# Kernel optimization log

Hardware: AMD Instinct MI355X
Metric: run time of the kernel (lower is better)

Reference implementation:

```python
import jax, jax.numpy as jnp
import numpy as np

EPS = 1e-5
NUM_HEADS = 8

def _inorm(x):
    # InstanceNorm1d (affine=False): normalize over last (length) axis per (B, C)
    m = x.mean(axis=-1, keepdims=True)
    v = x.var(axis=-1, keepdims=True)  # biased variance, as torch instance norm
    return (x - m) * jax.lax.rsqrt(v + EPS)

def setup_inputs() -> dict:
    key = jax.random.key(0)
    ks = jax.random.split(key, 12)
    B, Nl, HW = 4, 1024, 4096
    Cl, Cv, Ck, Cval, Cout = 512, 512, 256, 256, 256
    w = lambda k, shape: (jax.random.normal(k, shape, jnp.float32) * 0.02)
    return {
        "l": jax.random.normal(ks[0], (B, Nl, Cl), jnp.float32),
        "x": jax.random.normal(ks[1], (B, HW, Cv), jnp.float32),
        "Wq": w(ks[2], (Ck, Cl)),   "bq": w(ks[3], (Ck,)),
        "Wk": w(ks[4], (Ck, Cv)),   "bk": w(ks[5], (Ck,)),
        "Wv": w(ks[6], (Cval, Cv)), "bv": w(ks[7], (Cval,)),
        "Ww": w(ks[8], (Cout, Cval)), "bw": w(ks[9], (Cout,)),
    }

def reference(l, x, Wq, bq, Wk, bk, Wv, bv, Ww, bw):
    H = NUM_HEADS
    Ck = Wq.shape[0]
    Cv = Wv.shape[0]
    dk, dv = Ck // H, Cv // H
    B, Nl, _ = l.shape
    HW = x.shape[1]

    # 1x1 Conv1d == per-position linear
    q = jnp.einsum('blc,kc->blk', l, Wq) + bq                     # [B, Nl, Ck]
    k = jnp.einsum('bnc,kc->bkn', x, Wk) + bk[None, :, None]      # [B, Ck, HW]
    k = _inorm(k)                                                  # InstanceNorm over HW
    v = jnp.einsum('bnc,kc->bkn', x, Wv) + bv[None, :, None]      # [B, Cv, HW]

    q = q.reshape(B, Nl, H, dk).transpose(0, 2, 1, 3)             # [B, H, Nl, dk]
    k = k.reshape(B, H, dk, HW)                                   # [B, H, dk, HW]
    v = v.reshape(B, H, dv, HW)                                   # [B, H, dv, HW]

    sim = jnp.einsum('bhld,bhdn->bhln', q, k) * (Ck ** -0.5)      # [B, H, Nl, HW]
    att = jax.nn.softmax(sim, axis=-1)
    out = jnp.einsum('bhln,bhdn->bhld', att, v)                   # [B, H, Nl, dv]

    out = out.transpose(0, 2, 1, 3).reshape(B, Nl, Cv)            # [B, Nl, Cv]
    out = jnp.einsum('blc,oc->bol', out, Ww) + bw[None, :, None]  # [B, Cout, Nl]
    out = _inorm(out)                                              # InstanceNorm over Nl
    return out.transpose(0, 2, 1)                                  # [B, Nl, Cout]
```

## Files before the change

### kernel.cpp

```cpp
#include <hip/hip_runtime.h>

constexpr int Bn = 4, NL = 1024, HWn = 4096, NH = 8;

typedef __attribute__((ext_vector_type(8))) short bf16x8;
typedef __attribute__((ext_vector_type(4))) float f32x4;
#define MFMA16 __builtin_amdgcn_mfma_f32_16x16x32_bf16

extern "C" __device__ float __ocml_native_exp2_f32(float);

__device__ __forceinline__ float b2f(unsigned short u) {
  union { unsigned int i; float f; } x; x.i = ((unsigned int)u) << 16; return x.f;
}
__device__ __forceinline__ unsigned short f2b(float f) {
  union { float f; unsigned int i; } x; x.f = f;
  unsigned int r = x.i + 0x7fffu + ((x.i >> 16) & 1u);
  return (unsigned short)(r >> 16);
}

__device__ __forceinline__ void async_load16(const unsigned short* g, unsigned short* l) {
  __builtin_amdgcn_global_load_lds(
      (const __attribute__((address_space(1))) unsigned int*)g,
      (__attribute__((address_space(3))) unsigned int*)l, 16, 0, 0);
}

__global__ __launch_bounds__(256) void conv_bf16(const float* __restrict__ src,
    unsigned short* __restrict__ dst, int n)
{
  int i = (blockIdx.x * 256 + threadIdx.x) * 4;
  if (i < n) {
    float4 v = *(const float4*)(src + i);
    ushort4 o; o.x = f2b(v.x); o.y = f2b(v.y); o.z = f2b(v.z); o.w = f2b(v.w);
    *(ushort4*)(dst + i) = o;
  }
}

__global__ __launch_bounds__(256) void conv_w4(const float* __restrict__ Wk,
    const float* __restrict__ Wv, const float* __restrict__ Wq,
    const float* __restrict__ Ww,
    unsigned short* __restrict__ wkb, unsigned short* __restrict__ wvb,
    unsigned short* __restrict__ wqb,
    unsigned short* __restrict__ wwh, unsigned short* __restrict__ wwl)
{
  int i = (blockIdx.x * 256 + threadIdx.x) * 4;
  if (blockIdx.y == 3) {
    if (i >= 65536) return;
    float4 v = *(const float4*)(Ww + i);
    ushort4 hi, lo;
    hi.x = f2b(v.x); lo.x = f2b(v.x - b2f(hi.x));
    hi.y = f2b(v.y); lo.y = f2b(v.y - b2f(hi.y));
    hi.z = f2b(v.z); lo.z = f2b(v.z - b2f(hi.z));
    hi.w = f2b(v.w); lo.w = f2b(v.w - b2f(hi.w));
    *(ushort4*)(wwh + i) = hi;
    *(ushort4*)(wwl + i) = lo;
    return;
  }
  const float* src = blockIdx.y == 0 ? Wk : (blockIdx.y == 1 ? Wv : Wq);
  unsigned short* dst = blockIdx.y == 0 ? wkb : (blockIdx.y == 1 ? wvb : wqb);
  float4 v = *(const float4*)(src + i);
  ushort4 o; o.x = f2b(v.x); o.y = f2b(v.y); o.z = f2b(v.z); o.w = f2b(v.w);
  *(ushort4*)(dst + i) = o;
}

__global__ __launch_bounds__(256, 3) void gemm128(
    const unsigned short* __restrict__ xbf, const unsigned short* __restrict__ lbf,
    const unsigned short* __restrict__ wkb, const unsigned short* __restrict__ wvb,
    const unsigned short* __restrict__ wqb,
    const float* __restrict__ bk, const float* __restrict__ bv, const float* __restrict__ bq,
    unsigned short* __restrict__ khb, unsigned short* __restrict__ vhb,
    unsigned short* __restrict__ qbuf)
{
  __shared__ unsigned short As[2][4096];
  __shared__ unsigned short Bs[2][4096];
  const int id = blockIdx.x;
  const int mode = id < 256 ? 0 : (id < 512 ? 1 : 2);
  const int local = id - (mode == 0 ? 0 : (mode == 1 ? 256 : 512));
  const int rb = local >> 1, cb = local & 1;
  const int m0 = rb * 128, n0 = cb * 128;
  const unsigned short* A = (mode == 2) ? lbf : xbf;
  const unsigned short* W = (mode == 0) ? wkb : (mode == 1 ? wvb : wqb);
  const float* bias = (mode == 0) ? bk : (mode == 1 ? bv : bq);

  const int tid = threadIdx.x, w = tid >> 6, lane = tid & 63;
  const int quad = lane >> 4, l15 = lane & 15;
  const int wr = w >> 1, wc = w & 1;

  const int p0 = tid, p1 = tid + 256;
  const int am0 = p0 >> 2, ak0 = (p0 & 3) * 8;
  const int am1 = p1 >> 2, ak1 = (p1 & 3) * 8;

  f32x4 acc[4][4];
#pragma unroll
  for (int i = 0; i < 4; ++i)
#pragma unroll
    for (int j = 0; j < 4; ++j) acc[i][j] = (f32x4){0.f, 0.f, 0.f, 0.f};

  async_load16(A + (size_t)(m0 + am0) * 512 + ak0, &As[0][p0 * 8]);
  async_load16(A + (size_t)(m0 + am1) * 512 + ak1, &As[0][p1 * 8]);
  async_load16(W + (size_t)(n0 + am0) * 512 + ak0, &Bs[0][p0 * 8]);
  async_load16(W + (size_t)(n0 + am1) * 512 + ak1, &Bs[0][p1 * 8]);

  for (int kt = 0; kt < 16; ++kt) {
    const int cur = kt & 1;
    __syncthreads();
    if (kt < 15) {
      int k0 = (kt + 1) * 32;
      async_load16(A + (size_t)(m0 + am0) * 512 + k0 + ak0, &As[cur ^ 1][p0 * 8]);
      async_load16(A + (size_t)(m0 + am1) * 512 + k0 + ak1, &As[cur ^ 1][p1 * 8]);
      async_load16(W + (size_t)(n0 + am0) * 512 + k0 + ak0, &Bs[cur ^ 1][p0 * 8]);
      async_load16(W + (size_t)(n0 + am1) * 512 + k0 + ak1, &Bs[cur ^ 1][p1 * 8]);
    }
    bf16x8 af[4], bf[4];
#pragma unroll
    for (int fr = 0; fr < 4; ++fr)
      af[fr] = *(const bf16x8*)&As[cur][(wr * 64 + fr * 16 + l15) * 32 + quad * 8];
#pragma unroll
    for (int fc = 0; fc < 4; ++fc)
      bf[fc] = *(const bf16x8*)&Bs[cur][(wc * 64 + fc * 16 + l15) * 32 + quad * 8];
#pragma unroll
    for (int fr = 0; fr < 4; ++fr)
#pragma unroll
      for (int fc = 0; fc < 4; ++fc)
        acc[fr][fc] = MFMA16(af[fr], bf[fc], acc[fr][fc], 0, 0, 0);
  }

  float bb[4];
#pragma unroll
  for (int fc = 0; fc < 4; ++fc) bb[fc] = bias[n0 + wc * 64 + fc * 16 + l15];
  unsigned short* dst = (mode == 0) ? khb : (mode == 1 ? vhb : qbuf);
#pragma unroll
  for (int fr = 0; fr < 4; ++fr) {
#pragma unroll
    for (int fc = 0; fc < 4; ++fc) {
      int col = n0 + wc * 64 + fc * 16 + l15;
#pragma unroll
      for (int r = 0; r < 4; ++r) {
        int row = m0 + wr * 64 + fr * 16 + quad * 4 + r;
        unsigned short val = f2b(acc[fr][fc][r] + bb[fc]);
        if (mode == 2) {
          dst[(size_t)row * 256 + col] = val;
        } else {
          int b = row >> 12, n = row & 4095, h = col >> 5, d = col & 31;
          dst[((size_t)(b * 8 + h) * 4096 + n) * 32 + d] = val;
        }
      }
    }
  }
}

__global__ __launch_bounds__(256) void kvstats(const unsigned short* __restrict__ khb,
    const unsigned short* __restrict__ vhb,
    float* __restrict__ ksum, float* __restrict__ kss, float* __restrict__ vcs)
{
  const int which = blockIdx.x >> 5, bh = blockIdx.x & 31, seg = blockIdx.y;
  const int t = threadIdx.x, d = t & 31, g = t >> 5;
  __shared__ float rs[256], rss[256];
  if (which == 0) {
    const unsigned short* base = khb + (size_t)bh * 131072 + (size_t)seg * 512 * 32;
    float s = 0.f, ss = 0.f;
    for (int i = 0; i < 64; ++i) {
      float v = b2f(base[(size_t)(g + i * 8) * 32 + d]);
      s += v; ss += v * v;
    }
    rs[t] = s; rss[t] = ss;
    __syncthreads();
    if (t < 32) {
      float a = 0.f, b = 0.f;
      for (int g2 = 0; g2 < 8; ++g2) { a += rs[t + g2 * 32]; b += rss[t + g2 * 32]; }
      atomicAdd(&ksum[bh * 32 + t], a);
      atomicAdd(&kss[bh * 32 + t], b);
    }
  } else {
    const unsigned short* base = vhb + (size_t)bh * 131072 + (size_t)seg * 512 * 32;
    float s = 0.f;
    for (int i = 0; i < 64; ++i) s += b2f(base[(size_t)(g + i * 8) * 32 + d]);
    rs[t] = s;
    __syncthreads();
    if (t < 32) {
      float a = 0.f;
      for (int g2 = 0; g2 < 8; ++g2) a += rs[t + g2 * 32];
      vcs[seg * 1024 + bh * 32 + t] = a;
    }
  }
}

__global__ __launch_bounds__(256) void kfinal(const float* __restrict__ ksum,
    const float* __restrict__ kss, float* __restrict__ krstd)
{
  int i = blockIdx.x * 256 + threadIdx.x;
  float m = ksum[i] * (1.f / 4096.f);
  float var = kss[i] * (1.f / 4096.f) - m * m;
  krstd[i] = rsqrtf(var + 1e-5f);
}

__global__ __launch_bounds__(256) void vpack(const unsigned short* __restrict__ vh,
    unsigned short* __restrict__ vfrag)
{
  __shared__ unsigned short vt[256][42];
  const int bh = blockIdx.x >> 4, slab = blockIdx.x & 15;
  const unsigned short* src = vh + ((size_t)bh * 4096 + slab * 256) * 32;
  const int t = threadIdx.x;
#pragma unroll
  for (int i = 0; i < 4; ++i) {
    int p = i * 256 + t;
    int n = p >> 2, piece = p & 3;
    uint4 v = *(const uint4*)(src + (size_t)n * 32 + piece * 8);
    unsigned int* lrow = (unsigned int*)&vt[n][piece * 8];
    lrow[0] = v.x; lrow[1] = v.y; lrow[2] = v.z; lrow[3] = v.w;
  }
  __syncthreads();
#pragma unroll
  for (int i = 0; i < 4; ++i) {
    int op = i * 256 + t;
    int lanep = op & 63, rest = op >> 6;
    int dvt = rest & 1, kh2 = (rest >> 1) & 1, chunkl = rest >> 2;
    int lq = lanep >> 4, ll = lanep & 15;
    unsigned short o[8];
#pragma unroll
    for (int j = 0; j < 8; ++j) {
      int kappa = kh2 * 32 + lq * 8 + j;
      int nloc = (kappa >> 2) + 16 * (kappa & 3);
      o[j] = vt[chunkl * 64 + nloc][dvt * 16 + ll];
    }
    size_t dst = ((((size_t)bh * 64 + slab * 4 + chunkl) * 2 + kh2) * 2 + dvt) * 512 + lanep * 8;
    *(bf16x8*)(vfrag + dst) = *(const bf16x8*)o;
  }
}

__global__ __launch_bounds__(256, 4) void attn6(const unsigned short* __restrict__ qbuf,
    const unsigned short* __restrict__ khb, const unsigned short* __restrict__ vfrag,
    const float* __restrict__ krstd, const float* __restrict__ vcs,
    float* __restrict__ po, float* __restrict__ pd)
{
  const int bh = blockIdx.x, b = bh >> 3, h = bh & 7;
  const int lsuper = blockIdx.y, quarter = blockIdx.z;
  const int tid = threadIdx.x, w = tid >> 6, lane = tid & 63;
  const int quad = lane >> 4, l15 = lane & 15;

  __shared__ unsigned short kb_s[2][2048];
  __shared__ unsigned short vb_s[2][2048];
  __shared__ unsigned short ps[4][2][16][72];

  bf16x8 qa[2];
  {
    float fold[8];
    const float* rp = krstd + bh * 32 + quad * 8;
#pragma unroll
    for (int j = 0; j < 8; ++j) fold[j] = rp[j] * (0.0625f * 1.44269504f);
#pragma unroll
    for (int lf = 0; lf < 2; ++lf) {
      int l = lsuper * 128 + w * 32 + lf * 16 + l15;
      bf16x8 qr = *(const bf16x8*)(qbuf + ((size_t)(b * NL + l)) * 256 + h * 32 + quad * 8);
      const unsigned short* qq = (const unsigned short*)&qr;
      unsigned short tmp[8];
#pragma unroll
      for (int j = 0; j < 8; ++j) tmp[j] = f2b(b2f(qq[j]) * fold[j]);
      qa[lf] = *(const bf16x8*)tmp;
    }
  }

  float drow[2][4];
  f32x4 acc[2][2];
#pragma unroll
  for (int lf = 0; lf < 2; ++lf) {
#pragma unroll
    for (int r = 0; r < 4; ++r) drow[lf][r] = 0.f;
    acc[lf][0] = (f32x4){0.f,0.f,0.f,0.f};
    acc[lf][1] = (f32x4){0.f,0.f,0.f,0.f};
  }

  const unsigned short* kcbase = khb + (size_t)bh * 131072 + (size_t)quarter * 1024 * 32;
  const unsigned short* vcbase = vfrag + (size_t)bh * 131072 + (size_t)quarter * 16 * 2048;

  async_load16(kcbase + tid * 8, &kb_s[0][tid * 8]);
  async_load16(vcbase + tid * 8, &vb_s[0][tid * 8]);

  for (int c = 0; c < 16; ++c) {
    const int cur = c & 1;
    __syncthreads();
    if (c < 15) {
      async_load16(kcbase + (c + 1) * 2048 + tid * 8, &kb_s[cur ^ 1][tid * 8]);
      async_load16(vcbase + (c + 1) * 2048 + tid * 8, &vb_s[cur ^ 1][tid * 8]);
    }

    bf16x8 kb[4];
#pragma unroll
    for (int t = 0; t < 4; ++t)
      kb[t] = *(const bf16x8*)&kb_s[cur][(t * 16 + l15) * 32 + quad * 8];
    bf16x8 vb[4];
#pragma unroll
    for (int i = 0; i < 4; ++i)
      vb[i] = *(const bf16x8*)&vb_s[cur][i * 512 + lane * 8];

    f32x4 z = (f32x4){0.f,0.f,0.f,0.f};
#pragma unroll
    for (int lf = 0; lf < 2; ++lf) {
      f32x4 sv[4];
#pragma unroll
      for (int t = 0; t < 4; ++t) sv[t] = MFMA16(qa[lf], kb[t], z, 0, 0, 0);
#pragma unroll
      for (int r = 0; r < 4; ++r) {
        union { float f; unsigned int u; } e0, e1, e2, e3;
        float x0 = __ocml_native_exp2_f32(sv[0][r]);
        float x1 = __ocml_native_exp2_f32(sv[1][r]);
        float x2 = __ocml_native_exp2_f32(sv[2][r]);
        float x3 = __ocml_native_exp2_f32(sv[3][r]);
        drow[lf][r] += (x0 + x1) + (x2 + x3);
        e0.f = x0 - 1.0f; e1.f = x1 - 1.0f; e2.f = x2 - 1.0f; e3.f = x3 - 1.0f;
        uint2 pk;
        pk.x = (e0.u >> 16) | (e1.u & 0xFFFF0000u);
        pk.y = (e2.u >> 16) | (e3.u & 0xFFFF0000u);
        *(uint2*)&ps[w][lf][quad * 4 + r][l15 * 4] = pk;
      }
      asm volatile("s_waitcnt lgkmcnt(0)" ::: "memory");
#pragma unroll
      for (int kh2 = 0; kh2 < 2; ++kh2) {
        bf16x8 pa = *(const bf16x8*)&ps[w][lf][l15][kh2 * 32 + quad * 8];
#pragma unroll
        for (int dvt = 0; dvt < 2; ++dvt)
          acc[lf][dvt] = MFMA16(pa, vb[kh2 * 2 + dvt], acc[lf][dvt], 0, 0, 0);
      }
    }
  }

  const float* vc0 = vcs + (quarter * 2) * 1024 + bh * 32;
  const float* vc1 = vc0 + 1024;
  float cs0 = vc0[l15] + vc1[l15];
  float cs1 = vc0[16 + l15] + vc1[16 + l15];
#pragma unroll
  for (int lf = 0; lf < 2; ++lf)
#pragma unroll
    for (int r = 0; r < 4; ++r) {
      acc[lf][0][r] += cs0;
      acc[lf][1][r] += cs1;
    }

  const size_t PDo = (size_t)quarter * 32768 + (size_t)bh * 1024;
#pragma unroll
  for (int lf = 0; lf < 2; ++lf) {
#pragma unroll
    for (int r = 0; r < 4; ++r) {
      float sv = drow[lf][r];
      sv += __shfl_xor(sv, 1, 16);
      sv += __shfl_xor(sv, 2, 16);
      sv += __shfl_xor(sv, 4, 16);
      sv += __shfl_xor(sv, 8, 16);
      int l = lsuper * 128 + w * 32 + lf * 16 + quad * 4 + r;
      float2 val; val.x = acc[lf][0][r]; val.y = acc[lf][1][r];
      *(float2*)(po + (PDo + l) * 32 + l15 * 2) = val;
      if (l15 == 0) pd[PDo + l] = sv;
    }
  }
}

__global__ __launch_bounds__(256) void combine4(const float* __restrict__ po,
    const float* __restrict__ pd, unsigned short* __restrict__ aoh,
    unsigned short* __restrict__ aol)
{
  int gid = blockIdx.x * 256 + threadIdx.x;
  int dv = gid & 31, l = (gid >> 5) & (NL - 1), h = (gid >> 15) & 7, b = gid >> 18;
  int c = ((dv & 15) << 1) | (dv >> 4);
  size_t r = ((size_t)(b * 8 + h)) * 1024 + l;
  float d = 0.f, o = 0.f;
#pragma unroll
  for (int q = 0; q < 4; ++q) {
    size_t rr = (size_t)q * 32768 + r;
    d += pd[rr];
    o += po[rr * 32 + c];
  }
  o = o / d;
  unsigned short hi = f2b(o);
  size_t idx = ((size_t)(b * NL) + l) * 256 + h * 32 + dv;
  aoh[idx] = hi;
  aol[idx] = f2b(o - b2f(hi));
}

__global__ __launch_bounds__(256) void gemm_proj(
    const unsigned short* __restrict__ aoh, const unsigned short* __restrict__ aol,
    const unsigned short* __restrict__ wwh, const unsigned short* __restrict__ wwl,
    const float* __restrict__ bw, float* __restrict__ pj)
{
  __shared__ unsigned short As[64 * 32];
  __shared__ unsigned short Bs[128 * 32];
  const int bm = blockIdx.x * 64, bn = blockIdx.y * 128;
  const int tid = threadIdx.x, w = tid >> 6, lane = tid & 63;
  const int quad = lane >> 4, l15 = lane & 15;
  const int wr = w >> 1, wc = w & 1;
  const int arow = tid >> 2, apiece = (tid & 3) * 8;

  f32x4 acc[2][4];
#pragma unroll
  for (int i = 0; i < 2; ++i)
#pragma unroll
    for (int j = 0; j < 4; ++j) acc[i][j] = (f32x4){0.f, 0.f, 0.f, 0.f};

  for (int pair = 0; pair < 3; ++pair) {
    const unsigned short* A = (pair == 1) ? aol : aoh;
    const unsigned short* Bm = (pair == 2) ? wwl : wwh;
    for (int kt = 0; kt < 8; ++kt) {
      int k0 = kt * 32;
      __syncthreads();
      *(bf16x8*)&As[tid * 8] = *(const bf16x8*)(A + (size_t)(bm + arow) * 256 + k0 + apiece);
#pragma unroll
      for (int it = 0; it < 2; ++it) {
        int p = tid + it * 256;
        int brow = p >> 2, bpiece = (p & 3) * 8;
        *(bf16x8*)&Bs[p * 8] = *(const bf16x8*)(Bm + (size_t)(bn + brow) * 256 + k0 + bpiece);
      }
      __syncthreads();
      bf16x8 af[2], bf[4];
#pragma unroll
      for (int fr = 0; fr < 2; ++fr)
        af[fr] = *(const bf16x8*)&As[(wr * 32 + fr * 16 + l15) * 32 + quad * 8];
#pragma unroll
      for (int fc = 0; fc < 4; ++fc)
        bf[fc] = *(const bf16x8*)&Bs[(wc * 64 + fc * 16 + l15) * 32 + quad * 8];
#pragma unroll
      for (int fr = 0; fr < 2; ++fr)
#pragma unroll
        for (int fc = 0; fc < 4; ++fc)
          acc[fr][fc] = MFMA16(af[fr], bf[fc], acc[fr][fc], 0, 0, 0);
    }
  }

#pragma unroll
  for (int fr = 0; fr < 2; ++fr)
#pragma unroll
    for (int fc = 0; fc < 4; ++fc) {
      int col = bn + wc * 64 + fc * 16 + l15;
      float bb = bw[col];
#pragma unroll
      for (int r = 0; r < 4; ++r) {
        int row = bm + wr * 32 + fr * 16 + quad * 4 + r;
        pj[(size_t)row * 256 + col] = acc[fr][fc][r] + bb;
      }
    }
}

__global__ __launch_bounds__(256) void stats_kernel(const float* __restrict__ X,
    long batchStride, int rowsPerBlock,
    float* __restrict__ sum, float* __restrict__ sumsq)
{
  const int b = blockIdx.x, c = threadIdx.x;
  const long r0 = (long)blockIdx.y * rowsPerBlock;
  const float* base = X + (long)b * batchStride + r0 * 256 + c;
  float s = 0.f, ss = 0.f;
  for (int r = 0; r < rowsPerBlock; ++r) {
    float v = base[(long)r * 256];
    s += v; ss += v * v;
  }
  atomicAdd(&sum[b * 256 + c], s);
  atomicAdd(&sumsq[b * 256 + c], ss);
}

__global__ __launch_bounds__(256) void finalize_stats(const float* __restrict__ sum,
    const float* __restrict__ sumsq, float invR,
    float* __restrict__ mean, float* __restrict__ rstd)
{
  int i = blockIdx.x * 256 + threadIdx.x;
  float m = sum[i] * invR;
  float v = sumsq[i] * invR - m * m;
  mean[i] = m;
  rstd[i] = rsqrtf(v + 1e-5f);
}

__global__ __launch_bounds__(256) void final_out(const float* __restrict__ proj,
    const float* __restrict__ mean, const float* __restrict__ rstd,
    float* __restrict__ out)
{
  const int b = blockIdx.x, o = threadIdx.x;
  const int l1 = blockIdx.y * 16;
  const float m = mean[b * 256 + o], r = rstd[b * 256 + o];
  for (int i = 0; i < 16; ++i) {
    size_t idx = ((size_t)(b * NL + l1 + i)) * 256 + o;
    out[idx] = (proj[idx] - m) * r;
  }
}

extern "C" void kernel_launch(void* const* d_in, const int* in_sizes, int n_in,
                              void* d_out, int out_size, void* d_ws, size_t ws_size,
                              hipStream_t stream)
{
  const float* l  = (const float*)d_in[0];
  const float* x  = (const float*)d_in[1];
  const float* Wq = (const float*)d_in[2];
  const float* bq = (const float*)d_in[3];
  const float* Wk = (const float*)d_in[4];
  const float* bk = (const float*)d_in[5];
  const float* Wv = (const float*)d_in[6];
  const float* bv = (const float*)d_in[7];
  const float* Ww = (const float*)d_in[8];
  const float* bw = (const float*)d_in[9];
  float* out = (float*)d_out;

  unsigned short* up = (unsigned short*)d_ws;
  unsigned short* xbf   = up;
  unsigned short* lbf   = xbf   + 8388608;
  unsigned short* wkb   = lbf   + 2097152;
  unsigned short* wvb   = wkb   + 131072;
  unsigned short* wqb   = wvb   + 131072;
  unsigned short* qbuf  = wqb   + 131072;
  unsigned short* khb   = qbuf  + 1048576;
  unsigned short* vhb   = khb   + 4194304;
  unsigned short* vfrag = vhb   + 4194304;
  unsigned short* aoh   = vfrag + 4194304;
  unsigned short* aol   = aoh   + 1048576;
  unsigned short* wwh   = aol   + 1048576;
  unsigned short* wwl   = wwh   + 65536;
  float* F     = (float*)((char*)d_ws + 53477376);
  float* krstd = F;
  float* vcs   = krstd + 1024;
  float* po    = vcs + 8192;
  float* pd    = po + 4194304;
  float* pj    = pd + 131072;
  float* st    = pj + 1048576;
  float* ksum  = st;          float* kss   = st + 1024;
  float* psum  = st + 2048;   float* psq   = st + 3072;
  float* pmean = st + 4096;   float* prstd = st + 5120;

  hipMemsetAsync(st, 0, 4096 * sizeof(float), stream);

  dim3 blk(256);
  conv_bf16<<<8192, blk, 0, stream>>>(x,  xbf, 8388608);
  conv_bf16<<<2048, blk, 0, stream>>>(l,  lbf, 2097152);
  conv_w4<<<dim3(128, 4), blk, 0, stream>>>(Wk, Wv, Wq, Ww, wkb, wvb, wqb, wwh, wwl);
  gemm128<<<576, blk, 0, stream>>>(xbf, lbf, wkb, wvb, wqb, bk, bv, bq, khb, vhb, qbuf);
  kvstats<<<dim3(64, 8), blk, 0, stream>>>(khb, vhb, ksum, kss, vcs);
  kfinal<<<4, blk, 0, stream>>>(ksum, kss, krstd);
  vpack<<<512, blk, 0, stream>>>(vhb, vfrag);
  attn6<<<dim3(32, 8, 4), blk, 0, stream>>>(qbuf, khb, vfrag, krstd, vcs, po, pd);
  combine4<<<4096, blk, 0, stream>>>(po, pd, aoh, aol);
  gemm_proj<<<dim3(64, 2), blk, 0, stream>>>(aoh, aol, wwh, wwl, bw, pj);
  stats_kernel<<<dim3(4, 64), blk, 0, stream>>>(pj, (long)NL * 256, 16, psum, psq);
  finalize_stats<<<4, blk, 0, stream>>>(psum, psq, 1.0f / NL, pmean, prstd);
  final_out<<<dim3(4, 64), blk, 0, stream>>>(pj, pmean, prstd, out);
}
```

Measured before the change: 204.7 us.

## Fuse K/V and projection stats into GEMM epilogues; register-prefetch attention K/V

Moves the K sum/sumsq and V column-sum reductions into the gemm128 epilogue using wave shuffles and atomics, which removes the kvstats kernel and its re-read of khb/vhb. Likewise folds the output-projection instance-norm statistics into gemm_proj, removing stats_kernel. The attention kernel now loads K and V fragments straight from global memory into double-buffered registers instead of LDS with async copies and barriers. It also swizzles the P staging buffer and uses hardware packed bf16 conversion. Risks include extra atomic contention, higher register pressure in attention, and rounding differences from summing fp32 accumulators instead of bf16-rounded values.

Result: slower. 261.6 us (+27.8%).

```diff
diff --git a/kernel.cpp b/kernel.cpp
--- a/kernel.cpp
+++ b/kernel.cpp
@@ -67,7 +67,8 @@
     const unsigned short* __restrict__ wqb,
     const float* __restrict__ bk, const float* __restrict__ bv, const float* __restrict__ bq,
     unsigned short* __restrict__ khb, unsigned short* __restrict__ vhb,
-    unsigned short* __restrict__ qbuf)
+    unsigned short* __restrict__ qbuf,
+    float* __restrict__ ksum, float* __restrict__ kss, float* __restrict__ vcs)
 {
   __shared__ unsigned short As[2][4096];
   __shared__ unsigned short Bs[2][4096];
@@ -126,6 +127,35 @@
   float bb[4];
 #pragma unroll
   for (int fc = 0; fc < 4; ++fc) bb[fc] = bias[n0 + wc * 64 + fc * 16 + l15];
+
+  if (mode != 2) {
+    const int b = m0 >> 12;
+    const int seg = (m0 & 4095) >> 9;
+#pragma unroll
+    for (int fc = 0; fc < 4; ++fc) {
+      float s = 0.f, ssq = 0.f;
+#pragma unroll
+      for (int fr = 0; fr < 4; ++fr)
+#pragma unroll
+        for (int r = 0; r < 4; ++r) {
+          float v = acc[fr][fc][r] + bb[fc];
+          s += v; ssq += v * v;
+        }
+      s += __shfl_xor(s, 16); s += __shfl_xor(s, 32);
+      if (mode == 0) {
+        ssq += __shfl_xor(ssq, 16); ssq += __shfl_xor(ssq, 32);
+        if (quad == 0) {
+          int col = n0 + wc * 64 + fc * 16 + l15;
+          atomicAdd(&ksum[b * 256 + col], s);
+          atomicAdd(&kss[b * 256 + col], ssq);
+        }
+      } else if (quad == 0) {
+        int col = n0 + wc * 64 + fc * 16 + l15;
+        atomicAdd(&vcs[seg * 1024 + b * 256 + col], s);
+      }
+    }
+  }
+
   unsigned short* dst = (mode == 0) ? khb : (mode == 1 ? vhb : qbuf);
 #pragma unroll
   for (int fr = 0; fr < 4; ++fr) {
@@ -147,42 +177,6 @@
   }
 }
 
-__global__ __launch_bounds__(256) void kvstats(const unsigned short* __restrict__ khb,
-    const unsigned short* __restrict__ vhb,
-    float* __restrict__ ksum, float* __restrict__ kss, float* __restrict__ vcs)
-{
-  const int which = blockIdx.x >> 5, bh = blockIdx.x & 31, seg = blockIdx.y;
-  const int t = threadIdx.x, d = t & 31, g = t >> 5;
-  __shared__ float rs[256], rss[256];
-  if (which == 0) {
-    const unsigned short* base = khb + (size_t)bh * 131072 + (size_t)seg * 512 * 32;
-    float s = 0.f, ss = 0.f;
-    for (int i = 0; i < 64; ++i) {
-      float v = b2f(base[(size_t)(g + i * 8) * 32 + d]);
-      s += v; ss += v * v;
-    }
-    rs[t] = s; rss[t] = ss;
-    __syncthreads();
-    if (t < 32) {
-      float a = 0.f, b = 0.f;
-      for (int g2 = 0; g2 < 8; ++g2) { a += rs[t + g2 * 32]; b += rss[t + g2 * 32]; }
-      atomicAdd(&ksum[bh * 32 + t], a);
-      atomicAdd(&kss[bh * 32 + t], b);
-    }
-  } else {
-    const unsigned short* base = vhb + (size_t)bh * 131072 + (size_t)seg * 512 * 32;
-    float s = 0.f;
-    for (int i = 0; i < 64; ++i) s += b2f(base[(size_t)(g + i * 8) * 32 + d]);
-    rs[t] = s;
-    __syncthreads();
-    if (t < 32) {
-      float a = 0.f;
-      for (int g2 = 0; g2 < 8; ++g2) a += rs[t + g2 * 32];
-      vcs[seg * 1024 + bh * 32 + t] = a;
-    }
-  }
-}
-
 __global__ __launch_bounds__(256) void kfinal(const float* __restrict__ ksum,
     const float* __restrict__ kss, float* __restrict__ krstd)
 {
@@ -226,7 +220,7 @@
   }
 }
 
-__global__ __launch_bounds__(256, 4) void attn6(const unsigned short* __restrict__ qbuf,
+__global__ __launch_bounds__(256, 4) void attn7(const unsigned short* __restrict__ qbuf,
     const unsigned short* __restrict__ khb, const unsigned short* __restrict__ vfrag,
     const float* __restrict__ krstd, const float* __restrict__ vcs,
     float* __restrict__ po, float* __restrict__ pd)
@@ -236,9 +230,7 @@
   const int tid = threadIdx.x, w = tid >> 6, lane = tid & 63;
   const int quad = lane >> 4, l15 = lane & 15;
 
-  __shared__ unsigned short kb_s[2][2048];
-  __shared__ unsigned short vb_s[2][2048];
-  __shared__ unsigned short ps[4][2][16][72];
+  __shared__ unsigned short ps[4][2][16][64];
 
   bf16x8 qa[2];
   {
@@ -268,30 +260,28 @@
     acc[lf][1] = (f32x4){0.f,0.f,0.f,0.f};
   }
 
-  const unsigned short* kcbase = khb + (size_t)bh * 131072 + (size_t)quarter * 1024 * 32;
-  const unsigned short* vcbase = vfrag + (size_t)bh * 131072 + (size_t)quarter * 16 * 2048;
-
-  async_load16(kcbase + tid * 8, &kb_s[0][tid * 8]);
-  async_load16(vcbase + tid * 8, &vb_s[0][tid * 8]);
-
-  for (int c = 0; c < 16; ++c) {
-    const int cur = c & 1;
-    __syncthreads();
+  const unsigned short* kla = khb + (size_t)bh * 131072 + (size_t)quarter * 32768
+                              + l15 * 32 + quad * 8;
+  const unsigned short* vla = vfrag + (size_t)bh * 131072 + (size_t)quarter * 32768
+                              + lane * 8;
+
+  bf16x8 kbA[4], vbA[4], kbB[4], vbB[4];
+#pragma unroll
+  for (int t = 0; t < 4; ++t) kbA[t] = *(const bf16x8*)(kla + t * 512);
+#pragma unroll
+  for (int i = 0; i < 4; ++i) vbA[i] = *(const bf16x8*)(vla + i * 512);
+
+  unsigned short* psw = &ps[w][0][0][0];
+  const unsigned rdswz = (unsigned)((l15 & 7) << 4);
+
+  auto body = [&](bf16x8 (&kb)[4], bf16x8 (&vb)[4],
+                  bf16x8 (&kbN)[4], bf16x8 (&vbN)[4], int c) {
     if (c < 15) {
-      async_load16(kcbase + (c + 1) * 2048 + tid * 8, &kb_s[cur ^ 1][tid * 8]);
-      async_load16(vcbase + (c + 1) * 2048 + tid * 8, &vb_s[cur ^ 1][tid * 8]);
-    }
-
-    bf16x8 kb[4];
-#pragma unroll
-    for (int t = 0; t < 4; ++t)
-      kb[t] = *(const bf16x8*)&kb_s[cur][(t * 16 + l15) * 32 + quad * 8];
-    bf16x8 vb[4];
-#pragma unroll
-    for (int i = 0; i < 4; ++i)
-      vb[i] = *(const bf16x8*)&vb_s[cur][i * 512 + lane * 8];
-
-    f32x4 z = (f32x4){0.f,0.f,0.f,0.f};
+#pragma unroll
+      for (int t = 0; t < 4; ++t)
+        kbN[t] = *(const bf16x8*)(kla + (c + 1) * 2048 + t * 512);
+    }
+    const f32x4 z = (f32x4){0.f,0.f,0.f,0.f};
 #pragma unroll
     for (int lf = 0; lf < 2; ++lf) {
       f32x4 sv[4];
@@ -299,27 +289,41 @@
       for (int t = 0; t < 4; ++t) sv[t] = MFMA16(qa[lf], kb[t], z, 0, 0, 0);
 #pragma unroll
       for (int r = 0; r < 4; ++r) {
-        union { float f; unsigned int u; } e0, e1, e2, e3;
         float x0 = __ocml_native_exp2_f32(sv[0][r]);
         float x1 = __ocml_native_exp2_f32(sv[1][r]);
         float x2 = __ocml_native_exp2_f32(sv[2][r]);
         float x3 = __ocml_native_exp2_f32(sv[3][r]);
         drow[lf][r] += (x0 + x1) + (x2 + x3);
-        e0.f = x0 - 1.0f; e1.f = x1 - 1.0f; e2.f = x2 - 1.0f; e3.f = x3 - 1.0f;
-        uint2 pk;
-        pk.x = (e0.u >> 16) | (e1.u & 0xFFFF0000u);
-        pk.y = (e2.u >> 16) | (e3.u & 0xFFFF0000u);
-        *(uint2*)&ps[w][lf][quad * 4 + r][l15 * 4] = pk;
-      }
-      asm volatile("s_waitcnt lgkmcnt(0)" ::: "memory");
+        unsigned pk0, pk1;
+        asm("v_cvt_pk_bf16_f32 %0, %1, %2" : "=v"(pk0) : "v"(x0 - 1.0f), "v"(x1 - 1.0f));
+        asm("v_cvt_pk_bf16_f32 %0, %1, %2" : "=v"(pk1) : "v"(x2 - 1.0f), "v"(x3 - 1.0f));
+        const int row = quad * 4 + r;
+        unsigned off = (unsigned)((l15 * 8) ^ ((row & 7) << 4));
+        uint2 pk; pk.x = pk0; pk.y = pk1;
+        *(uint2*)((char*)(psw + lf * 1024 + row * 64) + off) = pk;
+      }
+    }
+    asm volatile("s_waitcnt lgkmcnt(0)" ::: "memory");
+#pragma unroll
+    for (int lf = 0; lf < 2; ++lf) {
 #pragma unroll
       for (int kh2 = 0; kh2 < 2; ++kh2) {
-        bf16x8 pa = *(const bf16x8*)&ps[w][lf][l15][kh2 * 32 + quad * 8];
-#pragma unroll
-        for (int dvt = 0; dvt < 2; ++dvt)
-          acc[lf][dvt] = MFMA16(pa, vb[kh2 * 2 + dvt], acc[lf][dvt], 0, 0, 0);
-      }
-    }
+        unsigned off = (unsigned)((kh2 * 64 + quad * 16) ^ rdswz);
+        bf16x8 pa = *(const bf16x8*)((const char*)(psw + lf * 1024 + l15 * 64) + off);
+        acc[lf][0] = MFMA16(pa, vb[kh2 * 2 + 0], acc[lf][0], 0, 0, 0);
+        acc[lf][1] = MFMA16(pa, vb[kh2 * 2 + 1], acc[lf][1], 0, 0, 0);
+      }
+    }
+    if (c < 15) {
+#pragma unroll
+      for (int i = 0; i < 4; ++i)
+        vbN[i] = *(const bf16x8*)(vla + (c + 1) * 2048 + i * 512);
+    }
+  };
+
+  for (int c = 0; c < 16; c += 2) {
+    body(kbA, vbA, kbB, vbB, c);
+    body(kbB, vbB, kbA, vbA, c + 1);
   }
 
   const float* vc0 = vcs + (quarter * 2) * 1024 + bh * 32;
@@ -377,7 +381,8 @@
 __global__ __launch_bounds__(256) void gemm_proj(
     const unsigned short* __restrict__ aoh, const unsigned short* __restrict__ aol,
     const unsigned short* __restrict__ wwh, const unsigned short* __restrict__ wwl,
-    const float* __restrict__ bw, float* __restrict__ pj)
+    const float* __restrict__ bw, float* __restrict__ pj,
+    float* __restrict__ psum, float* __restrict__ psq)
 {
   __shared__ unsigned short As[64 * 32];
   __shared__ unsigned short Bs[128 * 32];
@@ -422,34 +427,28 @@
     }
   }
 
+  const int b = bm >> 10;
 #pragma unroll
   for (int fr = 0; fr < 2; ++fr)
 #pragma unroll
     for (int fc = 0; fc < 4; ++fc) {
       int col = bn + wc * 64 + fc * 16 + l15;
       float bb = bw[col];
+      float s = 0.f, ssq = 0.f;
 #pragma unroll
       for (int r = 0; r < 4; ++r) {
         int row = bm + wr * 32 + fr * 16 + quad * 4 + r;
-        pj[(size_t)row * 256 + col] = acc[fr][fc][r] + bb;
-      }
-    }
-}
-
-__global__ __launch_bounds__(256) void stats_kernel(const float* __restrict__ X,
-    long batchStride, int rowsPerBlock,
-    float* __restrict__ sum, float* __restrict__ sumsq)
-{
-  const int b = blockIdx.x, c = threadIdx.x;
-  const long r0 = (long)blockIdx.y * rowsPerBlock;
-  const float* base = X + (long)b * batchStride + r0 * 256 + c;
-  float s = 0.f, ss = 0.f;
-  for (int r = 0; r < rowsPerBlock; ++r) {
-    float v = base[(long)r * 256];
-    s += v; ss += v * v;
-  }
-  atomicAdd(&sum[b * 256 + c], s);
-  atomicAdd(&sumsq[b * 256 + c], ss);
+        float v = acc[fr][fc][r] + bb;
+        pj[(size_t)row * 256 + col] = v;
+        s += v; ssq += v * v;
+      }
+      s += __shfl_xor(s, 16); s += __shfl_xor(s, 32);
+      ssq += __shfl_xor(ssq, 16); ssq += __shfl_xor(ssq, 32);
+      if (quad == 0) {
+        atomicAdd(&psum[b * 256 + col], s);
+        atomicAdd(&psq[b * 256 + col], ssq);
+      }
+    }
 }
 
 __global__ __launch_bounds__(256) void finalize_stats(const float* __restrict__ sum,
@@ -507,30 +506,31 @@
   unsigned short* wwh   = aol   + 1048576;
   unsigned short* wwl   = wwh   + 65536;
   float* F     = (float*)((char*)d_ws + 53477376);
-  float* krstd = F;
-  float* vcs   = krstd + 1024;
-  float* po    = vcs + 8192;
+  float* ksum  = F;
+  float* kss   = F + 1024;
+  float* vcs   = F + 2048;
+  float* psum  = F + 10240;
+  float* psq   = F + 11264;
+  float* krstd = F + 12288;
+  float* pmean = F + 13312;
+  float* prstd = F + 14336;
+  float* po    = F + 15360;
   float* pd    = po + 4194304;
-  float* pj    = pd + 131072;
-  float* st    = pj + 1048576;
-  float* ksum  = st;          float* kss   = st + 1024;
-  float* psum  = st + 2048;   float* psq   = st + 3072;
-  float* pmean = st + 4096;   float* prstd = st + 5120;
-
-  hipMemsetAsync(st, 0, 4096 * sizeof(float), stream);
+  float* pj    = po;
+
+  hipMemsetAsync(F, 0, 12288 * sizeof(float), stream);
 
   dim3 blk(256);
   conv_bf16<<<8192, blk, 0, stream>>>(x,  xbf, 8388608);
   conv_bf16<<<2048, blk, 0, stream>>>(l,  lbf, 2097152);
   conv_w4<<<dim3(128, 4), blk, 0, stream>>>(Wk, Wv, Wq, Ww, wkb, wvb, wqb, wwh, wwl);
-  gemm128<<<576, blk, 0, stream>>>(xbf, lbf, wkb, wvb, wqb, bk, bv, bq, khb, vhb, qbuf);
-  kvstats<<<dim3(64, 8), blk, 0, stream>>>(khb, vhb, ksum, kss, vcs);
+  gemm128<<<576, blk, 0, stream>>>(xbf, lbf, wkb, wvb, wqb, bk, bv, bq,
+                                   khb, vhb, qbuf, ksum, kss, vcs);
   kfinal<<<4, blk, 0, stream>>>(ksum, kss, krstd);
   vpack<<<512, blk, 0, stream>>>(vhb, vfrag);
-  attn6<<<dim3(32, 8, 4), blk, 0, stream>>>(qbuf, khb, vfrag, krstd, vcs, po, pd);
+  attn7<<<dim3(32, 8, 4), blk, 0, stream>>>(qbuf, khb, vfrag, krstd, vcs, po, pd);
   combine4<<<4096, blk, 0, stream>>>(po, pd, aoh, aol);
-  gemm_proj<<<dim3(64, 2), blk, 0, stream>>>(aoh, aol, wwh, wwl, bw, pj);
-  stats_kernel<<<dim3(4, 64), blk, 0, stream>>>(pj, (long)NL * 256, 16, psum, psq);
+  gemm_proj<<<dim3(64, 2), blk, 0, stream>>>(aoh, aol, wwh, wwl, bw, pj, psum, psq);
   finalize_stats<<<4, blk, 0, stream>>>(psum, psq, 1.0f / NL, pmean, prstd);
   final_out<<<dim3(4, 64), blk, 0, stream>>>(pj, pmean, prstd, out);
 }
```
